# Kernel optimization log

Measured on AMD Instinct MI355X. Metric: run time of the kernel, lower is better.

## Reference

```python
import jax, jax.numpy as jnp
import numpy as np

WS, SHIFT = 4, 2
Z, H, W = 16, 32, 32
C, HEADS, MLP = 384, 12, 1536
B = 4
N = WS ** 3                      # tokens per 3D window = 64
NW = (Z // WS) * (H // WS) * (W // WS)  # windows per sample = 256
L = Z * H * W
HEAD_DIM = C // HEADS


def _rel_pos_index():
    # replicates meshgrid_3d (which reverses its args) + index arithmetic
    arrs = (np.arange(WS), np.arange(WS), np.arange(WS))  # already symmetric (cubic)
    grids = []
    for i in range(3):
        slc = [1, 1, 1]; slc[i] = WS
        a = arrs[i].reshape(slc)
        for j in range(3):
            if j != i:
                a = a.repeat(WS, axis=j)
        grids.append(a)
    coords = np.stack(grids).reshape(3, -1)            # [3, N]
    rel = coords[:, :, None] - coords[:, None, :]      # [3, N, N]
    rel = rel.transpose(1, 2, 0)                       # [N, N, 3]
    rel[:, :, 0] += WS - 1
    rel[:, :, 1] += WS - 1
    rel[:, :, 2] += WS - 1
    rel[:, :, 0] *= (2 * WS - 1) * (2 * WS - 1)
    rel[:, :, 1] *= 2 * WS - 1
    return rel.sum(-1)                                 # [N, N] ints in [0, (2ws-1)^3)


def _attn_mask():
    # shifted-window mask, exactly as in build()
    m = np.zeros((Z, H, W))
    sl = (slice(0, -WS), slice(-WS, -SHIFT), slice(-SHIFT, None))
    cnt = 0
    for z in sl:
        for h in sl:
            for w in sl:
                m[z, h, w] = cnt
                cnt += 1
    mw = m.reshape(Z // WS, WS, H // WS, WS, W // WS, WS)
    mw = mw.transpose(0, 2, 4, 1, 3, 5).reshape(-1, N)        # [nW, N]
    diff = mw[:, None, :] - mw[:, :, None]                    # [nW, N, N]
    return np.where(diff != 0, -100.0, 0.0).astype(np.float32)


REL_IDX = jnp.asarray(_rel_pos_index())
MASK = jnp.asarray(_attn_mask())


def _ln(x, g, b):
    mu = jnp.mean(x, -1, keepdims=True)
    var = jnp.mean((x - mu) ** 2, -1, keepdims=True)
    return (x - mu) / jnp.sqrt(var + 1e-5) * g + b


def setup_inputs() -> dict:
    key = jax.random.key(0)
    ks = jax.random.split(key, 16)
    s = 0.02
    return {
        "x": jax.random.normal(ks[0], (B, L, C), jnp.float32),
        "norm1_g": jnp.ones((C,), jnp.float32),
        "norm1_b": jnp.zeros((C,), jnp.float32),
        "qkv_w": jax.random.normal(ks[1], (C, 3 * C), jnp.float32) * s,
        "qkv_b": jnp.zeros((3 * C,), jnp.float32),
        "proj_w": jax.random.normal(ks[2], (C, C), jnp.float32) * s,
        "proj_b": jnp.zeros((C,), jnp.float32),
        "rel_bias": jax.random.normal(ks[3], ((2 * WS - 1) ** 3, HEADS), jnp.float32) * s,
        "norm2_g": jnp.ones((C,), jnp.float32),
        "norm2_b": jnp.zeros((C,), jnp.float32),
        "fc1_w": jax.random.normal(ks[4], (C, MLP), jnp.float32) * s,
        "fc1_b": jnp.zeros((MLP,), jnp.float32),
        "fc2_w": jax.random.normal(ks[5], (MLP, C), jnp.float32) * s,
        "fc2_b": jnp.zeros((C,), jnp.float32),
    }


def reference(x, norm1_g, norm1_b, qkv_w, qkv_b, proj_w, proj_b, rel_bias,
              norm2_g, norm2_b, fc1_w, fc1_b, fc2_w, fc2_b):
    b = x.shape[0]
    skip = x
    h = _ln(x, norm1_g, norm1_b).reshape(b, Z, H, W, C)
    h = jnp.roll(h, (-SHIFT, -SHIFT, -SHIFT), axis=(1, 2, 3))
    # window partition -> [b*nW, N, C]
    win = h.reshape(b, Z // WS, WS, H // WS, WS, W // WS, WS, C)
    win = win.transpose(0, 1, 3, 5, 2, 4, 6, 7).reshape(-1, N, C)
    # windowed multi-head attention
    qkv = (win @ qkv_w + qkv_b).reshape(-1, N, 3, HEADS, HEAD_DIM)
    qkv = qkv.transpose(2, 0, 3, 1, 4)                        # [3, bnW, h, N, d]
    q, k, v = qkv[0], qkv[1], qkv[2]
    scale = HEAD_DIM ** -0.5
    attn = jnp.einsum('whnd,whmd->whnm', q * scale, k)        # [bnW, h, N, N]
    bias = rel_bias[REL_IDX.reshape(-1)].reshape(N, N, HEADS).transpose(2, 0, 1)
    attn = attn + bias[None]
    attn = attn.reshape(b, NW, HEADS, N, N) + MASK[None, :, None]
    attn = jax.nn.softmax(attn, axis=-1).reshape(-1, HEADS, N, N)
    o = jnp.einsum('whnm,whmd->whnd', attn, v)
    o = o.transpose(0, 2, 1, 3).reshape(-1, N, C) @ proj_w + proj_b
    # window reverse + unshift
    o = o.reshape(b, Z // WS, H // WS, W // WS, WS, WS, WS, C)
    o = o.transpose(0, 1, 4, 2, 5, 3, 6, 7).reshape(b, Z, H, W, C)
    o = jnp.roll(o, (SHIFT, SHIFT, SHIFT), axis=(1, 2, 3)).reshape(b, L, C)
    x2 = skip + o
    m = _ln(x2, norm2_g, norm2_b)
    m = jax.nn.gelu(m @ fc1_w + fc1_b, approximate=False) @ fc2_w + fc2_b
    return x2 + m
```

## Files before the change

### kernel.cpp

```cpp
#include <hip/hip_runtime.h>
#include <hip/hip_bf16.h>
#include <cstdint>
#include <cmath>


typedef __attribute__((ext_vector_type(4))) float f32x4;
typedef __attribute__((ext_vector_type(8))) __bf16 bf16x8_t;

static __device__ __forceinline__ short f2bf(float f) {
  unsigned u = __builtin_bit_cast(unsigned, f);
  unsigned lsb = (u >> 16) & 1u;
  u += 0x7fffu + lsb;
  return (short)(u >> 16);
}

static __device__ __forceinline__ void gload_lds16(const short* g, short* l) {
  __builtin_amdgcn_global_load_lds(
      (const __attribute__((address_space(1))) void*)g,
      (__attribute__((address_space(3))) void*)l, 16, 0, 0);
}

static constexpr size_t OFF_Q    = 0;
static constexpr size_t OFF_K    = 50331648;
static constexpr size_t OFF_V    = 100663296;
static constexpr size_t OFF_HID  = 0;
static constexpr size_t OFF_WIN  = 201326592;
static constexpr size_t OFF_WQ   = OFF_WIN + 50331648;
static constexpr size_t OFF_WP   = OFF_WQ  + 884736;
static constexpr size_t OFF_W1   = OFF_WP  + 294912;
static constexpr size_t OFF_W2   = OFF_W1  + 1179648;

__global__ void k_w2bf_t(const float* __restrict__ w, short* __restrict__ wt,
                         int K, int N) {
  int idx = blockIdx.x * 256 + threadIdx.x;
  if (idx >= K * N) return;
  int k = idx / N, n = idx - k * N;
  wt[(size_t)n * K + k] = f2bf(w[idx]);
}

__global__ __launch_bounds__(256) void k_ln1_window(
    const float* __restrict__ x, const float* __restrict__ gw,
    const float* __restrict__ gb, short* __restrict__ win) {
  int slot = blockIdx.x * 4 + (threadIdx.x >> 6);
  int lane = threadIdx.x & 63;
  int widx = slot >> 6, n = slot & 63;
  int bidx = widx >> 8, wloc = widx & 255;
  int z = ((wloc >> 6) << 2) + (n >> 4);
  int h = (((wloc >> 3) & 7) << 2) + ((n >> 2) & 3);
  int w = ((wloc & 7) << 2) + (n & 3);
  int zs = (z + 2) & 15, hs = (h + 2) & 31, ws = (w + 2) & 31;
  const float* xp = x + ((size_t)bidx * 16384 + zs * 1024 + hs * 32 + ws) * 384;
  float2 u[3]; float s = 0.f, s2 = 0.f;
#pragma unroll
  for (int j = 0; j < 3; j++) {
    u[j] = *(const float2*)(xp + lane * 2 + j * 128);
    s += u[j].x + u[j].y; s2 += u[j].x * u[j].x + u[j].y * u[j].y;
  }
#pragma unroll
  for (int o = 1; o < 64; o <<= 1) { s += __shfl_xor(s, o); s2 += __shfl_xor(s2, o); }
  float mu = s * (1.f / 384.f);
  float rinv = rsqrtf(s2 * (1.f / 384.f) - mu * mu + 1e-5f);
  short* wp = win + (size_t)slot * 384;
#pragma unroll
  for (int j = 0; j < 3; j++) {
    int c = lane * 2 + j * 128;
    ushort2 o;
    o.x = (unsigned short)f2bf((u[j].x - mu) * rinv * gw[c] + gb[c]);
    o.y = (unsigned short)f2bf((u[j].y - mu) * rinv * gw[c + 1] + gb[c + 1]);
    *(ushort2*)(wp + c) = o;
  }
}

__global__ __launch_bounds__(256) void k_ln2(
    const float* __restrict__ x2, const float* __restrict__ gw,
    const float* __restrict__ gb, short* __restrict__ h2) {
  int t = blockIdx.x * 4 + (threadIdx.x >> 6);
  int lane = threadIdx.x & 63;
  const float* xp = x2 + (size_t)t * 384;
  float2 u[3]; float s = 0.f, s2 = 0.f;
#pragma unroll
  for (int j = 0; j < 3; j++) {
    u[j] = *(const float2*)(xp + lane * 2 + j * 128);
    s += u[j].x + u[j].y; s2 += u[j].x * u[j].x + u[j].y * u[j].y;
  }
#pragma unroll
  for (int o = 1; o < 64; o <<= 1) { s += __shfl_xor(s, o); s2 += __shfl_xor(s2, o); }
  float mu = s * (1.f / 384.f);
  float rinv = rsqrtf(s2 * (1.f / 384.f) - mu * mu + 1e-5f);
  short* hp = h2 + (size_t)t * 384;
#pragma unroll
  for (int j = 0; j < 3; j++) {
    int c = lane * 2 + j * 128;
    ushort2 o;
    o.x = (unsigned short)f2bf((u[j].x - mu) * rinv * gw[c] + gb[c]);
    o.y = (unsigned short)f2bf((u[j].y - mu) * rinv * gw[c + 1] + gb[c + 1]);
    *(ushort2*)(hp + c) = o;
  }
}

template <int EPI, int KDIM>
__global__ __launch_bounds__(256) void k_gemm(
    const short* __restrict__ A, const short* __restrict__ Bt,
    const float* __restrict__ bias, short* __restrict__ ob0,
    short* __restrict__ ob1, short* __restrict__ ob2,
    const float* __restrict__ aux, float* __restrict__ of32) {
  __shared__ short As[16384];
  __shared__ short Bs[16384];
  const int tid = threadIdx.x;
  const int wave = tid >> 6, lane = tid & 63;
  const int g = lane >> 4, li = lane & 15;

  const int nx = gridDim.x;
  const int nwg = nx * gridDim.y;
  int bid = blockIdx.y * nx + blockIdx.x;
  const int cpx = nwg >> 3;
  bid = (bid & 7) * cpx + (bid >> 3);
  const int m0 = (bid / nx) << 7, n0 = (bid % nx) << 7;

  const int srow = tid >> 3;
  const int sc8 = (tid & 7) ^ (srow & 7);
  const short* gA = A + (size_t)(m0 + srow) * KDIM + sc8 * 8;
  const short* gB = Bt + (size_t)(n0 + srow) * KDIM + sc8 * 8;
  short* lA = As + wave * 512;
  short* lB = Bs + wave * 512;

  const int wm = wave >> 1, wn = wave & 1;
  const int kx = (li & 7) << 3;
  const short* ra = As + (wm * 64 + li) * 64;
  const short* rb = Bs + (wn * 64 + li) * 64;
  const int c00 = (g * 8) ^ kx;
  const int c32 = (32 + g * 8) ^ kx;

  f32x4 acc[4][4] = {};

#define STAGE(buf, kt)                                                        \
  do {                                                                        \
    _Pragma("unroll") for (int p = 0; p < 4; p++) {                           \
      gload_lds16(gA + (size_t)(p * 32) * KDIM + (kt),                        \
                  lA + (buf) * 8192 + p * 2048);                              \
      gload_lds16(gB + (size_t)(p * 32) * KDIM + (kt),                        \
                  lB + (buf) * 8192 + p * 2048);                              \
    }                                                                         \
  } while (0)

#define COMPUTE(buf)                                                          \
  do {                                                                        \
    const short* ra_ = ra + (buf) * 8192;                                     \
    const short* rb_ = rb + (buf) * 8192;                                     \
    bf16x8_t a0[4], a1[4], b0[4], b1[4];                                      \
    _Pragma("unroll") for (int i = 0; i < 4; i++) {                           \
      a0[i] = *(const bf16x8_t*)(ra_ + i * 1024 + c00);                       \
      a1[i] = *(const bf16x8_t*)(ra_ + i * 1024 + c32);                       \
      b0[i] = *(const bf16x8_t*)(rb_ + i * 1024 + c00);                       \
      b1[i] = *(const bf16x8_t*)(rb_ + i * 1024 + c32);                       \
    }                                                                         \
    _Pragma("unroll") for (int mi = 0; mi < 4; mi++)                          \
        _Pragma("unroll") for (int ni = 0; ni < 4; ni++) acc[mi][ni] =        \
        __builtin_amdgcn_mfma_f32_16x16x32_bf16(a0[mi], b0[ni], acc[mi][ni],  \
                                                0, 0, 0);                     \
    _Pragma("unroll") for (int mi = 0; mi < 4; mi++)                          \
        _Pragma("unroll") for (int ni = 0; ni < 4; ni++) acc[mi][ni] =        \
        __builtin_amdgcn_mfma_f32_16x16x32_bf16(a1[mi], b1[ni], acc[mi][ni],  \
                                                0, 0, 0);                     \
  } while (0)

  constexpr int NT = KDIM / 64;
  STAGE(0, 0);
  asm volatile("s_waitcnt vmcnt(0)" ::: "memory");
  __syncthreads();
  int cur = 0;
  for (int t = 0; t < NT - 1; ++t) {
    STAGE(cur ^ 1, (t + 1) * 64);
    COMPUTE(cur);
    asm volatile("s_waitcnt vmcnt(0)" ::: "memory");
    __syncthreads();
    cur ^= 1;
  }
  COMPUTE(cur);
#undef STAGE
#undef COMPUTE

#pragma unroll
  for (int mi = 0; mi < 4; mi++) {
#pragma unroll
    for (int ni = 0; ni < 4; ni++) {
      const int col = n0 + wn * 64 + ni * 16 + li;
      const float bc = bias[col];
      const int rbase = m0 + wm * 64 + mi * 16 + g * 4;
      if constexpr (EPI == 0) {
        const int s = col / 384;
        const int rem = col - s * 384;
        const int head = rem >> 5, d = rem & 31;
#pragma unroll
        for (int r = 0; r < 4; r++) {
          const int row = rbase + r;
          const int widx = row >> 6, n = row & 63;
          float v = acc[mi][ni][r] + bc;
          if (s == 0)
            ob0[(((size_t)widx * 12 + head) * 64 + n) * 32 + d] =
                f2bf(v * 0.17677669529663687f);
          else if (s == 1)
            ob1[(((size_t)widx * 12 + head) * 64 + n) * 32 + d] = f2bf(v);
          else
            ob2[(((size_t)widx * 12 + head) * 32 + d) * 64 + n] = f2bf(v);
        }
      } else if constexpr (EPI == 1) {
#pragma unroll
        for (int r = 0; r < 4; r++) {
          const int row = rbase + r;
          const int widx = row >> 6, n = row & 63;
          const int wloc = widx & 255, bb = widx >> 8;
          const int z = ((wloc >> 6) << 2) + (n >> 4);
          const int h = (((wloc >> 3) & 7) << 2) + ((n >> 2) & 3);
          const int w = ((wloc & 7) << 2) + (n & 3);
          const int zs = (z + 2) & 15, hs = (h + 2) & 31, wsx = (w + 2) & 31;
          const size_t t = (size_t)bb * 16384 + zs * 1024 + hs * 32 + wsx;
          of32[t * 384 + col] = aux[t * 384 + col] + acc[mi][ni][r] + bc;
        }
      } else if constexpr (EPI == 2) {
#pragma unroll
        for (int r = 0; r < 4; r++) {
          const int row = rbase + r;
          float v = acc[mi][ni][r] + bc;
          ob0[(size_t)row * 1536 + col] =
              f2bf(0.5f * v * (1.f + erff(v * 0.70710678118654752f)));
        }
      } else {
#pragma unroll
        for (int r = 0; r < 4; r++) {
          const int row = rbase + r;
          of32[(size_t)row * 384 + col] =
              aux[(size_t)row * 384 + col] + acc[mi][ni][r] + bc;
        }
      }
    }
  }
}

__global__ __launch_bounds__(256) void k_attn(
    const short* __restrict__ qb, const short* __restrict__ kb,
    const short* __restrict__ vb, const float* __restrict__ relb,
    short* __restrict__ owin) {
  __shared__ short pt[4][5120];
  const int wave = threadIdx.x >> 6;
  const int wh_ = blockIdx.x * 4 + wave;
  const int widx = wh_ / 12, head = wh_ - widx * 12;
  const int lane = threadIdx.x & 63;
  const int g = lane >> 4, li = lane & 15;
  const short* qp = qb + (size_t)wh_ * 2048;
  const short* kp = kb + (size_t)wh_ * 2048;
  const short* vp = vb + (size_t)wh_ * 2048;
  short* ptw = pt[wave];
  bf16x8_t kf[4], qf[4];
#pragma unroll
  for (int t = 0; t < 4; t++) {
    kf[t] = *(const bf16x8_t*)(kp + (t * 16 + li) * 32 + g * 8);
    qf[t] = *(const bf16x8_t*)(qp + (t * 16 + li) * 32 + g * 8);
  }
  f32x4 zero = {0.f, 0.f, 0.f, 0.f};
  f32x4 st[4][4];
#pragma unroll
  for (int ti = 0; ti < 4; ti++)
#pragma unroll
    for (int tj = 0; tj < 4; tj++)
      st[ti][tj] = __builtin_amdgcn_mfma_f32_16x16x32_bf16(kf[ti], qf[tj], zero, 0, 0, 0);
  const int wloc = widx & 255;
  const int wz = wloc >> 6, wh2 = (wloc >> 3) & 7, ww2 = wloc & 7;
#pragma unroll
  for (int tj = 0; tj < 4; tj++) {
    const int qn = tj * 16 + li;
    const int qz = qn >> 4, qh = (qn >> 2) & 3, qw = qn & 3;
    const int cq = ((wz < 3) ? 0 : ((qz < 2) ? 1 : 2)) * 9 +
                   ((wh2 < 7) ? 0 : ((qh < 2) ? 1 : 2)) * 3 +
                   ((ww2 < 7) ? 0 : ((qw < 2) ? 1 : 2));
    float mx = -1e30f;
#pragma unroll
    for (int ti = 0; ti < 4; ti++) {
#pragma unroll
      for (int r = 0; r < 4; r++) {
        const int kn = ti * 16 + g * 4 + r;
        const int kz = kn >> 4, kh = (kn >> 2) & 3, kw = kn & 3;
        const int ck = ((wz < 3) ? 0 : ((kz < 2) ? 1 : 2)) * 9 +
                       ((wh2 < 7) ? 0 : ((kh < 2) ? 1 : 2)) * 3 +
                       ((ww2 < 7) ? 0 : ((kw < 2) ? 1 : 2));
        const int idx = (qz - kz + 3) * 49 + (qh - kh + 3) * 7 + (qw - kw + 3);
        float v = st[ti][tj][r] + relb[idx * 12 + head] + ((ck == cq) ? 0.f : -100.f);
        st[ti][tj][r] = v;
        mx = fmaxf(mx, v);
      }
    }
    mx = fmaxf(mx, __shfl_xor(mx, 16));
    mx = fmaxf(mx, __shfl_xor(mx, 32));
    float sum = 0.f;
#pragma unroll
    for (int ti = 0; ti < 4; ti++)
#pragma unroll
      for (int r = 0; r < 4; r++) {
        float e = __expf(st[ti][tj][r] - mx);
        st[ti][tj][r] = e;
        sum += e;
      }
    sum += __shfl_xor(sum, 16);
    sum += __shfl_xor(sum, 32);
    const float rs = 1.f / sum;
#pragma unroll
    for (int ti = 0; ti < 4; ti++)
#pragma unroll
      for (int r = 0; r < 4; r++)
        ptw[qn * 80 + ti * 16 + g * 4 + r] = f2bf(st[ti][tj][r] * rs);
  }
  __syncthreads();
  f32x4 o[4][2] = {};
#pragma unroll
  for (int kb2 = 0; kb2 < 2; kb2++) {
    bf16x8_t pa[4], bv[2];
#pragma unroll
    for (int tq = 0; tq < 4; tq++)
      pa[tq] = *(const bf16x8_t*)(ptw + (tq * 16 + li) * 80 + kb2 * 32 + g * 8);
#pragma unroll
    for (int td = 0; td < 2; td++)
      bv[td] = *(const bf16x8_t*)(vp + (td * 16 + li) * 64 + kb2 * 32 + g * 8);
#pragma unroll
    for (int tq = 0; tq < 4; tq++)
#pragma unroll
      for (int td = 0; td < 2; td++)
        o[tq][td] = __builtin_amdgcn_mfma_f32_16x16x32_bf16(pa[tq], bv[td], o[tq][td], 0, 0, 0);
  }
#pragma unroll
  for (int tq = 0; tq < 4; tq++)
#pragma unroll
    for (int td = 0; td < 2; td++)
#pragma unroll
      for (int r = 0; r < 4; r++) {
        const int qn = tq * 16 + g * 4 + r;
        const int d = td * 16 + li;
        owin[((size_t)widx * 64 + qn) * 384 + head * 32 + d] = f2bf(o[tq][td][r]);
      }
}

extern "C" void kernel_launch(void* const* d_in, const int* in_sizes, int n_in,
                              void* d_out, int out_size, void* d_ws,
                              size_t ws_size, hipStream_t stream) {
  (void)in_sizes; (void)n_in; (void)out_size; (void)ws_size;
  const float* x      = (const float*)d_in[0];
  const float* n1g    = (const float*)d_in[1];
  const float* n1b    = (const float*)d_in[2];
  const float* qkv_w  = (const float*)d_in[3];
  const float* qkv_b  = (const float*)d_in[4];
  const float* proj_w = (const float*)d_in[5];
  const float* proj_b = (const float*)d_in[6];
  const float* relb   = (const float*)d_in[7];
  const float* n2g    = (const float*)d_in[8];
  const float* n2b    = (const float*)d_in[9];
  const float* fc1_w  = (const float*)d_in[10];
  const float* fc1_b  = (const float*)d_in[11];
  const float* fc2_w  = (const float*)d_in[12];
  const float* fc2_b  = (const float*)d_in[13];
  float* out = (float*)d_out;
  char* ws = (char*)d_ws;

  short* qbuf = (short*)(ws + OFF_Q);
  short* kbuf = (short*)(ws + OFF_K);
  short* vbuf = (short*)(ws + OFF_V);
  short* hid  = (short*)(ws + OFF_HID);
  short* win  = (short*)(ws + OFF_WIN);
  short* owin = (short*)(ws + OFF_WIN);
  short* h2   = (short*)(ws + OFF_WIN);
  float* x2   = out;
  short* wq   = (short*)(ws + OFF_WQ);
  short* wp   = (short*)(ws + OFF_WP);
  short* w1   = (short*)(ws + OFF_W1);
  short* w2   = (short*)(ws + OFF_W2);

  k_w2bf_t<<<(384 * 1152 + 255) / 256, 256, 0, stream>>>(qkv_w, wq, 384, 1152);
  k_w2bf_t<<<(384 * 384 + 255) / 256, 256, 0, stream>>>(proj_w, wp, 384, 384);
  k_w2bf_t<<<(384 * 1536 + 255) / 256, 256, 0, stream>>>(fc1_w, w1, 384, 1536);
  k_w2bf_t<<<(1536 * 384 + 255) / 256, 256, 0, stream>>>(fc2_w, w2, 1536, 384);

  k_ln1_window<<<16384, 256, 0, stream>>>(x, n1g, n1b, win);
  k_gemm<0, 384><<<dim3(9, 512), 256, 0, stream>>>(win, wq, qkv_b, qbuf, kbuf,
                                                   vbuf, nullptr, nullptr);
  k_attn<<<3072, 256, 0, stream>>>(qbuf, kbuf, vbuf, relb, owin);
  k_gemm<1, 384><<<dim3(3, 512), 256, 0, stream>>>(owin, wp, proj_b, nullptr,
                                                   nullptr, nullptr, x, x2);
  k_ln2<<<16384, 256, 0, stream>>>(x2, n2g, n2b, h2);
  k_gemm<2, 384><<<dim3(12, 512), 256, 0, stream>>>(h2, w1, fc1_b, hid, nullptr,
                                                    nullptr, nullptr, nullptr);
  k_gemm<3, 1536><<<dim3(3, 512), 256, 0, stream>>>(hid, w2, fc2_b, nullptr,
                                                    nullptr, nullptr, x2, out);
}
```

Before: 805.0 us.

## Use 256x128 GEMM tiles with 3-stage K=32 LDS pipeline

The GEMM tile grows from 128x128 to 256x128, so each wave now holds 8x4 accumulators and the grid's M dimension is halved. The K step shrinks from 64 to 32 and the two-buffer loop becomes a three-buffer pipeline, with partial vmcnt waits that keep two stages of global-to-LDS loads in flight. The LDS swizzle layout is reworked to match the new tile shape, and launch bounds now request 2 blocks per CU. The aim is more data reuse per loaded tile and better hiding of load latency. The cost is higher register pressure from 128 accumulator floats per lane, two barriers per K step, and fewer workgroups per launch.

```diff
diff --git a/kernel.cpp b/kernel.cpp
--- a/kernel.cpp
+++ b/kernel.cpp
@@ -99,13 +99,13 @@
 }
 
 template <int EPI, int KDIM>
-__global__ __launch_bounds__(256) void k_gemm(
+__global__ __launch_bounds__(256, 2) void k_gemm(
     const short* __restrict__ A, const short* __restrict__ Bt,
     const float* __restrict__ bias, short* __restrict__ ob0,
     short* __restrict__ ob1, short* __restrict__ ob2,
     const float* __restrict__ aux, float* __restrict__ of32) {
-  __shared__ short As[16384];
-  __shared__ short Bs[16384];
+  __shared__ short As[24576];
+  __shared__ short Bs[12288];
   const int tid = threadIdx.x;
   const int wave = tid >> 6, lane = tid & 63;
   const int g = lane >> 4, li = lane & 15;
@@ -115,78 +115,79 @@
   int bid = blockIdx.y * nx + blockIdx.x;
   const int cpx = nwg >> 3;
   bid = (bid & 7) * cpx + (bid >> 3);
-  const int m0 = (bid / nx) << 7, n0 = (bid % nx) << 7;
-
-  const int srow = tid >> 3;
-  const int sc8 = (tid & 7) ^ (srow & 7);
-  const short* gA = A + (size_t)(m0 + srow) * KDIM + sc8 * 8;
-  const short* gB = Bt + (size_t)(n0 + srow) * KDIM + sc8 * 8;
-  short* lA = As + wave * 512;
-  short* lB = Bs + wave * 512;
+  const int m0 = (bid / nx) << 8, n0 = (bid % nx) << 7;
+
+  const int u_ = tid >> 3;
+  const int s_ = tid & 7;
+  const int sx = s_ ^ (u_ & 7);
+  const int srow = (u_ << 1) + (sx >> 2);
+  const int scol = (sx & 3) << 3;
+  const short* gAs = A + (size_t)(m0 + srow) * KDIM + scol;
+  const short* gBs = Bt + (size_t)(n0 + srow) * KDIM + scol;
+  short* lAs = As + wave * 512;
+  short* lBs = Bs + wave * 512;
 
   const int wm = wave >> 1, wn = wave & 1;
-  const int kx = (li & 7) << 3;
-  const short* ra = As + (wm * 64 + li) * 64;
-  const short* rb = Bs + (wn * 64 + li) * 64;
-  const int c00 = (g * 8) ^ kx;
-  const int c32 = (32 + g * 8) ^ kx;
-
-  f32x4 acc[4][4] = {};
+  const int li2 = li >> 1;
+  const int slot = (((li & 1) << 2) + g) ^ li2;
+  const int abase = wm * 4096 + li2 * 64 + slot * 8;
+  const int bbase = wn * 2048 + li2 * 64 + slot * 8;
+
+  f32x4 acc[8][4] = {};
 
 #define STAGE(buf, kt)                                                        \
   do {                                                                        \
-    _Pragma("unroll") for (int p = 0; p < 4; p++) {                           \
-      gload_lds16(gA + (size_t)(p * 32) * KDIM + (kt),                        \
-                  lA + (buf) * 8192 + p * 2048);                              \
-      gload_lds16(gB + (size_t)(p * 32) * KDIM + (kt),                        \
-                  lB + (buf) * 8192 + p * 2048);                              \
-    }                                                                         \
+    _Pragma("unroll") for (int p = 0; p < 4; p++)                             \
+        gload_lds16(gAs + (size_t)(p * 64) * KDIM + (kt),                     \
+                    lAs + (buf) * 8192 + p * 2048);                           \
+    _Pragma("unroll") for (int p = 0; p < 2; p++)                             \
+        gload_lds16(gBs + (size_t)(p * 64) * KDIM + (kt),                     \
+                    lBs + (buf) * 4096 + p * 2048);                           \
   } while (0)
 
 #define COMPUTE(buf)                                                          \
   do {                                                                        \
-    const short* ra_ = ra + (buf) * 8192;                                     \
-    const short* rb_ = rb + (buf) * 8192;                                     \
-    bf16x8_t a0[4], a1[4], b0[4], b1[4];                                      \
-    _Pragma("unroll") for (int i = 0; i < 4; i++) {                           \
-      a0[i] = *(const bf16x8_t*)(ra_ + i * 1024 + c00);                       \
-      a1[i] = *(const bf16x8_t*)(ra_ + i * 1024 + c32);                       \
-      b0[i] = *(const bf16x8_t*)(rb_ + i * 1024 + c00);                       \
-      b1[i] = *(const bf16x8_t*)(rb_ + i * 1024 + c32);                       \
-    }                                                                         \
-    _Pragma("unroll") for (int mi = 0; mi < 4; mi++)                          \
+    const short* pa = As + (buf) * 8192 + abase;                              \
+    const short* pb = Bs + (buf) * 4096 + bbase;                              \
+    bf16x8_t a[8], b[4];                                                      \
+    _Pragma("unroll") for (int mi = 0; mi < 8; mi++)                          \
+        a[mi] = *(const bf16x8_t*)(pa + mi * 512);                            \
+    _Pragma("unroll") for (int ni = 0; ni < 4; ni++)                          \
+        b[ni] = *(const bf16x8_t*)(pb + ni * 512);                            \
+    _Pragma("unroll") for (int mi = 0; mi < 8; mi++)                          \
         _Pragma("unroll") for (int ni = 0; ni < 4; ni++) acc[mi][ni] =        \
-        __builtin_amdgcn_mfma_f32_16x16x32_bf16(a0[mi], b0[ni], acc[mi][ni],  \
-                                                0, 0, 0);                     \
-    _Pragma("unroll") for (int mi = 0; mi < 4; mi++)                          \
-        _Pragma("unroll") for (int ni = 0; ni < 4; ni++) acc[mi][ni] =        \
-        __builtin_amdgcn_mfma_f32_16x16x32_bf16(a1[mi], b1[ni], acc[mi][ni],  \
+        __builtin_amdgcn_mfma_f32_16x16x32_bf16(a[mi], b[ni], acc[mi][ni],    \
                                                 0, 0, 0);                     \
   } while (0)
 
-  constexpr int NT = KDIM / 64;
+  constexpr int NT = KDIM / 32;
   STAGE(0, 0);
-  asm volatile("s_waitcnt vmcnt(0)" ::: "memory");
-  __syncthreads();
-  int cur = 0;
-  for (int t = 0; t < NT - 1; ++t) {
-    STAGE(cur ^ 1, (t + 1) * 64);
-    COMPUTE(cur);
-    asm volatile("s_waitcnt vmcnt(0)" ::: "memory");
-    __syncthreads();
-    cur ^= 1;
-  }
-  COMPUTE(cur);
+  STAGE(1, 32);
+#pragma unroll 3
+  for (int t = 0; t < NT; ++t) {
+    asm volatile("s_waitcnt lgkmcnt(0)" ::: "memory");
+    __builtin_amdgcn_s_barrier();
+    if (t + 2 < NT) {
+      STAGE((t + 2) % 3, (t + 2) * 32);
+      asm volatile("s_waitcnt vmcnt(12)" ::: "memory");
+    } else if (t + 1 < NT) {
+      asm volatile("s_waitcnt vmcnt(6)" ::: "memory");
+    } else {
+      asm volatile("s_waitcnt vmcnt(0)" ::: "memory");
+    }
+    __builtin_amdgcn_s_barrier();
+    COMPUTE(t % 3);
+  }
 #undef STAGE
 #undef COMPUTE
 
 #pragma unroll
-  for (int mi = 0; mi < 4; mi++) {
+  for (int mi = 0; mi < 8; mi++) {
 #pragma unroll
     for (int ni = 0; ni < 4; ni++) {
       const int col = n0 + wn * 64 + ni * 16 + li;
       const float bc = bias[col];
-      const int rbase = m0 + wm * 64 + mi * 16 + g * 4;
+      const int rbase = m0 + wm * 128 + mi * 16 + g * 4;
       if constexpr (EPI == 0) {
         const int s = col / 384;
         const int rem = col - s * 384;
@@ -378,14 +379,14 @@
   k_w2bf_t<<<(1536 * 384 + 255) / 256, 256, 0, stream>>>(fc2_w, w2, 1536, 384);
 
   k_ln1_window<<<16384, 256, 0, stream>>>(x, n1g, n1b, win);
-  k_gemm<0, 384><<<dim3(9, 512), 256, 0, stream>>>(win, wq, qkv_b, qbuf, kbuf,
+  k_gemm<0, 384><<<dim3(9, 256), 256, 0, stream>>>(win, wq, qkv_b, qbuf, kbuf,
                                                    vbuf, nullptr, nullptr);
   k_attn<<<3072, 256, 0, stream>>>(qbuf, kbuf, vbuf, relb, owin);
-  k_gemm<1, 384><<<dim3(3, 512), 256, 0, stream>>>(owin, wp, proj_b, nullptr,
+  k_gemm<1, 384><<<dim3(3, 256), 256, 0, stream>>>(owin, wp, proj_b, nullptr,
                                                    nullptr, nullptr, x, x2);
   k_ln2<<<16384, 256, 0, stream>>>(x2, n2g, n2b, h2);
-  k_gemm<2, 384><<<dim3(12, 512), 256, 0, stream>>>(h2, w1, fc1_b, hid, nullptr,
+  k_gemm<2, 384><<<dim3(12, 256), 256, 0, stream>>>(h2, w1, fc1_b, hid, nullptr,
                                                     nullptr, nullptr, nullptr);
-  k_gemm<3, 1536><<<dim3(3, 512), 256, 0, stream>>>(hid, w2, fc2_b, nullptr,
+  k_gemm<3, 1536><<<dim3(3, 256), 256, 0, stream>>>(hid, w2, fc2_b, nullptr,
                                                     nullptr, nullptr, x2, out);
 }
```

Result: no change. 799.0 us (-0.7%).
